# Kernel optimization log

Hardware: AMD Instinct MI355X
Metric: run time of the kernel (lower is better)

The kernel has to match this reference:

```python
import jax, jax.numpy as jnp
import numpy as np

B, D, NSTEPS = 256, 4096, 30
DT = 0.5  # args.dt

def rho(x):
    # hard-sigmoid activation used throughout the EP repo
    return jnp.clip(x, 0.0, 1.0)

def setup_inputs() -> dict:
    key = jax.random.key(0)
    k_s3, k_w0, k_w2, k_w4 = jax.random.split(key, 4)
    sc = 1.0 / np.sqrt(D)
    W0 = jax.random.normal(k_w0, (D, D), jnp.float32) * sc  # w[0]: layer1 -> layer0
    W2 = jax.random.normal(k_w2, (D, D), jnp.float32) * sc  # w[2]: layer2 -> layer1
    W4 = jax.random.normal(k_w4, (D, D), jnp.float32) * sc  # w[4]: data  -> layer2
    return {
        "s0": jnp.zeros((B, D), jnp.float32),
        "s1": jnp.zeros((B, D), jnp.float32),
        "s2": jnp.zeros((B, D), jnp.float32),
        "s3": jax.random.uniform(k_s3, (B, D), jnp.float32),  # clamped data layer in [0,1]
        "W0": W0, "b0": jnp.zeros((D,), jnp.float32),
        "W1": W0.T,  # w[2i+1].weight = w[2i].weight.T at init (tied transpose)
        "W2": W2, "b2": jnp.zeros((D,), jnp.float32),
        "W3": W2.T,
        "W4": W4, "b4": jnp.zeros((D,), jnp.float32),
        "N": NSTEPS,
    }

def reference(s0, s1, s2, s3, W0, b0, W1, W2, b2, W3, W4, b4, N):
    # non-spiking EP free-phase relaxation (beta=0), no_clamp=False
    top_in = rho(s3) @ W4.T + b4  # s3 is clamped data; constant across steps

    def step(carry, _):
        c0, c1, c2 = carry
        r0, r1, r2 = rho(c0), rho(c1), rho(c2)
        ds0 = -c0 + r1 @ W0.T + b0
        ds1 = -c1 + r2 @ W2.T + b2 + r0 @ W1.T
        ds2 = -c2 + top_in + r1 @ W3.T
        n0 = jnp.clip(c0 + DT * ds0, 0.0, 1.0)
        n1 = jnp.clip(c1 + DT * ds1, 0.0, 1.0)
        n2 = jnp.clip(c2 + DT * ds2, 0.0, 1.0)
        return (n0, n1, n2), None

    (s0, s1, s2), _ = jax.lax.scan(step, (s0, s1, s2), None, length=N)
    return jnp.stack([s0, s1, s2])  # [3, B, D]
```

## Files before the change

kernel.cpp:

```cpp
#include <hip/hip_runtime.h>


typedef unsigned short u16;
typedef __attribute__((ext_vector_type(8))) _Float16 f16x8;
typedef __attribute__((ext_vector_type(4))) float f32x4;

constexpr int Bb = 256, Dd = 4096, NSTEPS = 30;
constexpr long BD = (long)Bb * Dd;
constexpr long DD = (long)Dd * Dd;
constexpr int BM = 32;
constexpr int NBUF = 3;
constexpr int BUFB = 20480;

__device__ inline u16 f2h(float f) { union { _Float16 h; u16 u; } v; v.h = (_Float16)f; return v.u; }
__device__ inline float h2f(u16 b) { union { u16 u; _Float16 h; } v; v.u = b; return (float)v.h; }

__device__ inline void gl_lds16(const u16* g, void* l) {
    __builtin_amdgcn_global_load_lds(
        (const __attribute__((address_space(1))) void*)g,
        (__attribute__((address_space(3))) void*)l, 16, 0, 0);
}

__global__ __launch_bounds__(256)
void convert_w(const float* __restrict__ src, u16* __restrict__ dst, long n) {
    long i = (long)blockIdx.x * blockDim.x + threadIdx.x;
    const long stride = (long)gridDim.x * blockDim.x;
    for (long v = i; v < (n >> 2); v += stride) {
        float4 x = ((const float4*)src)[v];
        ushort4 o; o.x = f2h(x.x); o.y = f2h(x.y); o.z = f2h(x.z); o.w = f2h(x.w);
        ((ushort4*)dst)[v] = o;
    }
}

__global__ __launch_bounds__(256)
void convert_s(const float* __restrict__ src, u16* __restrict__ hi, u16* __restrict__ lo, long n) {
    long i = (long)blockIdx.x * blockDim.x + threadIdx.x;
    const long stride = (long)gridDim.x * blockDim.x;
    for (long v = i; v < (n >> 2); v += stride) {
        float4 x = ((const float4*)src)[v];
        float a[4] = {x.x, x.y, x.z, x.w};
        ushort4 oh, ol;
        u16* ph = (u16*)&oh; u16* pl = (u16*)&ol;
        #pragma unroll
        for (int j = 0; j < 4; ++j) {
            float c = fminf(fmaxf(a[j], 0.f), 1.f);
            u16 hb = f2h(c);
            ph[j] = hb;
            pl[j] = f2h(c - h2f(hb));
        }
        ((ushort4*)hi)[v] = oh;
        ((ushort4*)lo)[v] = ol;
    }
}

template<bool WIDE>
__device__ inline void stage_tile(const u16* aH, const u16* aL, const u16* W,
                                  int m0, int n0, int k, char* buf, int wv, int lane)
{
    const int srow = lane >> 2;
    const int koff = (((lane & 3) ^ ((lane >> 3) & 3)) << 3);
    const u16* aBase = (wv < 2) ? aH : aL;
    const int aRow = ((wv & 1) << 4) + srow;
    char* aDst = buf + ((wv >> 1) << 11) + ((wv & 1) << 10);
    gl_lds16(aBase + (size_t)(m0 + aRow) * Dd + k + koff, aDst);
    constexpr int WR = WIDE ? 64 : 32;
    const u16* wSrc = W + (size_t)(n0 + WR * wv + srow) * Dd + k + koff;
    char* wDst = buf + 4096 + wv * (WIDE ? 4096 : 2048);
    #pragma unroll
    for (int c = 0; c < (WIDE ? 4 : 2); ++c)
        gl_lds16(wSrc + (size_t)(16 * c) * Dd, wDst + (c << 10));
}

template<int MODE, bool WIDE>
__device__ inline void run_gemm(const u16* aH0, const u16* aL0, const u16* W0p,
                                const u16* aH1, const u16* aL1, const u16* W1p,
                                const int npass, const int m0, const int n0, char* smem,
                                const float* bias, const float* add,
                                const float* pF, const u16* pH, const u16* pL,
                                float* outF, u16* oH, u16* oL, const long zOff)
{
    const int lane = threadIdx.x & 63, wv = threadIdx.x >> 6;
    constexpr int NJ = WIDE ? 4 : 2;
    f32x4 acc[2][NJ] = {};
    const int nk = npass << 7;

    stage_tile<WIDE>(aH0, aL0, W0p, m0, n0, 0,  smem,        wv, lane);
    stage_tile<WIDE>(aH0, aL0, W0p, m0, n0, 32, smem + BUFB, wv, lane);

    int ib = 0;
    const int r16 = lane & 15;
    const int qoff = (((lane >> 4) ^ ((r16 >> 1) & 3)) << 4);

    for (int kk = 0; kk < nk; ++kk) {
        if (kk + 1 < nk) {
            if (WIDE) asm volatile("s_waitcnt vmcnt(5)" ::: "memory");
            else      asm volatile("s_waitcnt vmcnt(3)" ::: "memory");
        } else {
            asm volatile("s_waitcnt vmcnt(0)" ::: "memory");
        }
        __builtin_amdgcn_s_barrier();
        asm volatile("" ::: "memory");

        const int kk2 = kk + 2;
        if (kk2 < nk) {
            int ib2 = ib + 2; if (ib2 >= NBUF) ib2 -= NBUF;
            const bool p1 = kk2 >= 128;
            stage_tile<WIDE>(p1 ? aH1 : aH0, p1 ? aL1 : aL0, p1 ? W1p : W0p,
                             m0, n0, (kk2 & 127) << 5, smem + ib2 * BUFB, wv, lane);
        }

        const char* buf = smem + ib * BUFB;
        ++ib; if (ib == NBUF) ib = 0;

        f16x8 ah[2], al[2], wf[NJ];
        #pragma unroll
        for (int i = 0; i < 2; ++i) {
            ah[i] = *(const f16x8*)(buf + ((16 * i + r16) << 6) + qoff);
            al[i] = *(const f16x8*)(buf + 2048 + ((16 * i + r16) << 6) + qoff);
        }
        #pragma unroll
        for (int j = 0; j < NJ; ++j)
            wf[j] = *(const f16x8*)(buf + 4096 +
                        (((WIDE ? 64 : 32) * wv + 16 * j + r16) << 6) + qoff);

        __builtin_amdgcn_s_setprio(1);
        #pragma unroll
        for (int j = 0; j < NJ; ++j) {
            #pragma unroll
            for (int i = 0; i < 2; ++i) {
                acc[i][j] = __builtin_amdgcn_mfma_f32_16x16x32_f16(ah[i], wf[j], acc[i][j], 0, 0, 0);
                acc[i][j] = __builtin_amdgcn_mfma_f32_16x16x32_f16(al[i], wf[j], acc[i][j], 0, 0, 0);
            }
        }
        __builtin_amdgcn_s_setprio(0);
    }

    const int q = lane >> 4;
    #pragma unroll
    for (int j = 0; j < NJ; ++j) {
        const int n = n0 + (WIDE ? 64 : 32) * wv + 16 * j + r16;
        #pragma unroll
        for (int i = 0; i < 2; ++i) {
            #pragma unroll
            for (int r = 0; r < 4; ++r) {
                const int m = m0 + 16 * i + q * 4 + r;
                const size_t idx = (size_t)m * Dd + n;
                float e = acc[i][j][r];
                if (MODE == 0) {
                    outF[idx] = e + bias[n];
                } else {
                    if (bias) e += bias[n];
                    if (add)  e += add[idx];
                    const float p = pF ? pF[zOff + idx] : (h2f(pH[zOff + idx]) + h2f(pL[zOff + idx]));
                    float v = 0.5f * p + 0.5f * e;
                    v = fminf(fmaxf(v, 0.f), 1.f);
                    const u16 hb = f2h(v);
                    oH[zOff + idx] = hb;
                    oL[zOff + idx] = f2h(v - h2f(hb));
                    if (outF) outF[zOff + idx] = v;
                }
            }
        }
    }
}

template<int MODE>
__global__ __launch_bounds__(256, 2)
void step_mfma(const u16* __restrict__ sH, const u16* __restrict__ sL,
               const u16* __restrict__ W0h, const u16* __restrict__ W1h,
               const u16* __restrict__ W2h, const u16* __restrict__ W3h,
               const float* __restrict__ b0, const float* __restrict__ b2,
               const float* __restrict__ top,
               const float* __restrict__ pF,
               const u16* __restrict__ pH, const u16* __restrict__ pL,
               float* __restrict__ outF,
               u16* __restrict__ oH, u16* __restrict__ oL)
{
    __shared__ __align__(16) char smem[NBUF * BUFB];
    const int id = blockIdx.x;

    if (MODE == 0) {
        const int mt = id >> 5, nt = id & 31;
        run_gemm<0, false>(sH, sL, W0h, nullptr, nullptr, nullptr, 1,
                           mt * BM, nt * 128, smem, b0, nullptr,
                           nullptr, nullptr, nullptr, outF, nullptr, nullptr, 0);
    } else {
        if (id < 128) {
            const int mt = id >> 4, nt = id & 15;
            run_gemm<1, true>(sH + BD, sL + BD, W0h, nullptr, nullptr, nullptr, 1,
                              mt * BM, nt * 256, smem, b0, nullptr,
                              pF, pH, pL, outF, oH, oL, 0);
        } else if (id < 384) {
            const int t = id - 128, mt = t >> 5, nt = t & 31;
            run_gemm<1, false>(sH + 2 * BD, sL + 2 * BD, W2h, sH, sL, W1h, 2,
                               mt * BM, nt * 128, smem, b2, nullptr,
                               pF, pH, pL, outF, oH, oL, BD);
        } else {
            const int t = id - 384, mt = t >> 4, nt = t & 15;
            run_gemm<1, true>(sH + BD, sL + BD, W3h, nullptr, nullptr, nullptr, 1,
                              mt * BM, nt * 256, smem, nullptr, top,
                              pF, pH, pL, outF, oH, oL, 2 * BD);
        }
    }
}

extern "C" void kernel_launch(void* const* d_in, const int* in_sizes, int n_in,
                              void* d_out, int out_size, void* d_ws, size_t ws_size,
                              hipStream_t stream)
{
    const float* s0 = (const float*)d_in[0];
    const float* s1 = (const float*)d_in[1];
    const float* s2 = (const float*)d_in[2];
    const float* s3 = (const float*)d_in[3];
    const float* W0 = (const float*)d_in[4];
    const float* b0 = (const float*)d_in[5];
    const float* W1 = (const float*)d_in[6];
    const float* W2 = (const float*)d_in[7];
    const float* b2 = (const float*)d_in[8];
    const float* W3 = (const float*)d_in[9];
    const float* W4 = (const float*)d_in[10];
    const float* b4 = (const float*)d_in[11];

    float* top = (float*)d_ws;
    u16* u   = (u16*)(top + BD);
    u16* W0h = u;            u16* W1h = u + DD;     u16* W2h = u + 2 * DD;
    u16* W3h = u + 3 * DD;   u16* W4h = u + 4 * DD;
    u16* sHa = u + 5 * DD;
    u16* sLa = sHa + 3 * BD;
    u16* sHb = sLa + 3 * BD;
    u16* sLb = sHb + 3 * BD;
    u16* s3h = sLb + 3 * BD;
    u16* s3l = s3h + BD;

    float* out = (float*)d_out;
    const dim3 blk(256);
    const dim3 cgrid(512);

    convert_w<<<cgrid, blk, 0, stream>>>(W0, W0h, DD);
    convert_w<<<cgrid, blk, 0, stream>>>(W1, W1h, DD);
    convert_w<<<cgrid, blk, 0, stream>>>(W2, W2h, DD);
    convert_w<<<cgrid, blk, 0, stream>>>(W3, W3h, DD);
    convert_w<<<cgrid, blk, 0, stream>>>(W4, W4h, DD);
    convert_s<<<cgrid, blk, 0, stream>>>(s3, s3h, s3l, BD);
    convert_s<<<cgrid, blk, 0, stream>>>(s0, sHa,          sLa,          BD);
    convert_s<<<cgrid, blk, 0, stream>>>(s1, sHa + BD,     sLa + BD,     BD);
    convert_s<<<cgrid, blk, 0, stream>>>(s2, sHa + 2 * BD, sLa + 2 * BD, BD);

    step_mfma<0><<<dim3(256), blk, 0, stream>>>(
        s3h, s3l, W4h, nullptr, nullptr, nullptr,
        b4, nullptr, nullptr,
        nullptr, nullptr, nullptr,
        top, nullptr, nullptr);

    for (int t = 0; t < NSTEPS; ++t) {
        const u16* iH = (t & 1) ? sHb : sHa;
        const u16* iL = (t & 1) ? sLb : sLa;
        u16*       vH = (t & 1) ? sHa : sHb;
        u16*       vL = (t & 1) ? sLa : sLb;
        float* oF = (t == NSTEPS - 1) ? out : nullptr;
        if (t == 0) {
            hipMemcpyAsync(out,          s0, BD * sizeof(float), hipMemcpyDeviceToDevice, stream);
            hipMemcpyAsync(out + BD,     s1, BD * sizeof(float), hipMemcpyDeviceToDevice, stream);
            hipMemcpyAsync(out + 2 * BD, s2, BD * sizeof(float), hipMemcpyDeviceToDevice, stream);
            step_mfma<1><<<dim3(512), blk, 0, stream>>>(
                iH, iL, W0h, W1h, W2h, W3h, b0, b2, top,
                out, nullptr, nullptr,
                oF, vH, vL);
        } else {
            step_mfma<1><<<dim3(512), blk, 0, stream>>>(
                iH, iL, W0h, W1h, W2h, W3h, b0, b2, top,
                nullptr, iH, iL,
                oF, vH, vL);
        }
    }
}
```

Before: 3.760 ms.

## Split layer-1 two-pass GEMM into two wide tiles with separate finish kernel

The layer-1 update, which needed a K=8192 two-pass GEMM over narrow 128-column tiles, is split into two independent K=4096 GEMMs on wide 256-column tiles that write fp32 partials. A new elementwise kernel sums the partials and applies the update, clamp and hi/lo split. All blocks now do equal work, which removes the long tail from the double-length layer-1 blocks, and the wider tiles reuse the A operand more. In exchange it adds a kernel launch per step plus extra global traffic for the partials. The partials reuse the W4 conversion buffer as scratch, and the top-input GEMM now also uses wide tiles.

```diff
diff --git a/kernel.cpp b/kernel.cpp
--- a/kernel.cpp
+++ b/kernel.cpp
@@ -53,7 +53,6 @@
     }
 }
 
-template<bool WIDE>
 __device__ inline void stage_tile(const u16* aH, const u16* aL, const u16* W,
                                   int m0, int n0, int k, char* buf, int wv, int lane)
 {
@@ -63,69 +62,58 @@
     const int aRow = ((wv & 1) << 4) + srow;
     char* aDst = buf + ((wv >> 1) << 11) + ((wv & 1) << 10);
     gl_lds16(aBase + (size_t)(m0 + aRow) * Dd + k + koff, aDst);
-    constexpr int WR = WIDE ? 64 : 32;
-    const u16* wSrc = W + (size_t)(n0 + WR * wv + srow) * Dd + k + koff;
-    char* wDst = buf + 4096 + wv * (WIDE ? 4096 : 2048);
+    const u16* wSrc = W + (size_t)(n0 + 64 * wv + srow) * Dd + k + koff;
+    char* wDst = buf + 4096 + wv * 4096;
     #pragma unroll
-    for (int c = 0; c < (WIDE ? 4 : 2); ++c)
+    for (int c = 0; c < 4; ++c)
         gl_lds16(wSrc + (size_t)(16 * c) * Dd, wDst + (c << 10));
 }
 
-template<int MODE, bool WIDE>
-__device__ inline void run_gemm(const u16* aH0, const u16* aL0, const u16* W0p,
-                                const u16* aH1, const u16* aL1, const u16* W1p,
-                                const int npass, const int m0, const int n0, char* smem,
+template<bool FULL>
+__device__ inline void run_gemm(const u16* aH, const u16* aL, const u16* W,
+                                const int m0, const int n0, char* smem,
                                 const float* bias, const float* add,
                                 const float* pF, const u16* pH, const u16* pL,
                                 float* outF, u16* oH, u16* oL, const long zOff)
 {
     const int lane = threadIdx.x & 63, wv = threadIdx.x >> 6;
-    constexpr int NJ = WIDE ? 4 : 2;
-    f32x4 acc[2][NJ] = {};
-    const int nk = npass << 7;
-
-    stage_tile<WIDE>(aH0, aL0, W0p, m0, n0, 0,  smem,        wv, lane);
-    stage_tile<WIDE>(aH0, aL0, W0p, m0, n0, 32, smem + BUFB, wv, lane);
+    f32x4 acc[2][4] = {};
+    constexpr int nk = 128;
+
+    stage_tile(aH, aL, W, m0, n0, 0,  smem,        wv, lane);
+    stage_tile(aH, aL, W, m0, n0, 32, smem + BUFB, wv, lane);
 
     int ib = 0;
     const int r16 = lane & 15;
     const int qoff = (((lane >> 4) ^ ((r16 >> 1) & 3)) << 4);
 
     for (int kk = 0; kk < nk; ++kk) {
-        if (kk + 1 < nk) {
-            if (WIDE) asm volatile("s_waitcnt vmcnt(5)" ::: "memory");
-            else      asm volatile("s_waitcnt vmcnt(3)" ::: "memory");
-        } else {
-            asm volatile("s_waitcnt vmcnt(0)" ::: "memory");
-        }
+        if (kk + 1 < nk) asm volatile("s_waitcnt vmcnt(5)" ::: "memory");
+        else             asm volatile("s_waitcnt vmcnt(0)" ::: "memory");
         __builtin_amdgcn_s_barrier();
         asm volatile("" ::: "memory");
 
-        const int kk2 = kk + 2;
-        if (kk2 < nk) {
+        if (kk + 2 < nk) {
             int ib2 = ib + 2; if (ib2 >= NBUF) ib2 -= NBUF;
-            const bool p1 = kk2 >= 128;
-            stage_tile<WIDE>(p1 ? aH1 : aH0, p1 ? aL1 : aL0, p1 ? W1p : W0p,
-                             m0, n0, (kk2 & 127) << 5, smem + ib2 * BUFB, wv, lane);
+            stage_tile(aH, aL, W, m0, n0, (kk + 2) << 5, smem + ib2 * BUFB, wv, lane);
         }
 
         const char* buf = smem + ib * BUFB;
         ++ib; if (ib == NBUF) ib = 0;
 
-        f16x8 ah[2], al[2], wf[NJ];
+        f16x8 ah[2], al[2], wf[4];
         #pragma unroll
         for (int i = 0; i < 2; ++i) {
             ah[i] = *(const f16x8*)(buf + ((16 * i + r16) << 6) + qoff);
             al[i] = *(const f16x8*)(buf + 2048 + ((16 * i + r16) << 6) + qoff);
         }
         #pragma unroll
-        for (int j = 0; j < NJ; ++j)
-            wf[j] = *(const f16x8*)(buf + 4096 +
-                        (((WIDE ? 64 : 32) * wv + 16 * j + r16) << 6) + qoff);
+        for (int j = 0; j < 4; ++j)
+            wf[j] = *(const f16x8*)(buf + 4096 + ((64 * wv + 16 * j + r16) << 6) + qoff);
 
         __builtin_amdgcn_s_setprio(1);
         #pragma unroll
-        for (int j = 0; j < NJ; ++j) {
+        for (int j = 0; j < 4; ++j) {
             #pragma unroll
             for (int i = 0; i < 2; ++i) {
                 acc[i][j] = __builtin_amdgcn_mfma_f32_16x16x32_f16(ah[i], wf[j], acc[i][j], 0, 0, 0);
@@ -137,8 +125,8 @@
 
     const int q = lane >> 4;
     #pragma unroll
-    for (int j = 0; j < NJ; ++j) {
-        const int n = n0 + (WIDE ? 64 : 32) * wv + 16 * j + r16;
+    for (int j = 0; j < 4; ++j) {
+        const int n = n0 + 64 * wv + 16 * j + r16;
         #pragma unroll
         for (int i = 0; i < 2; ++i) {
             #pragma unroll
@@ -146,8 +134,8 @@
                 const int m = m0 + 16 * i + q * 4 + r;
                 const size_t idx = (size_t)m * Dd + n;
                 float e = acc[i][j][r];
-                if (MODE == 0) {
-                    outF[idx] = e + bias[n];
+                if (!FULL) {
+                    outF[idx] = bias ? e + bias[n] : e;
                 } else {
                     if (bias) e += bias[n];
                     if (add)  e += add[idx];
@@ -174,34 +162,70 @@
                const float* __restrict__ pF,
                const u16* __restrict__ pH, const u16* __restrict__ pL,
                float* __restrict__ outF,
-               u16* __restrict__ oH, u16* __restrict__ oL)
+               u16* __restrict__ oH, u16* __restrict__ oL,
+               float* __restrict__ p0, float* __restrict__ p1)
 {
     __shared__ __align__(16) char smem[NBUF * BUFB];
     const int id = blockIdx.x;
 
     if (MODE == 0) {
-        const int mt = id >> 5, nt = id & 31;
-        run_gemm<0, false>(sH, sL, W0h, nullptr, nullptr, nullptr, 1,
-                           mt * BM, nt * 128, smem, b0, nullptr,
-                           nullptr, nullptr, nullptr, outF, nullptr, nullptr, 0);
+        const int mt = id >> 4, nt = id & 15;
+        run_gemm<false>(sH, sL, W0h, mt * BM, nt * 256, smem, b0, nullptr,
+                        nullptr, nullptr, nullptr, outF, nullptr, nullptr, 0);
     } else {
+        const int t = id & 127, mt = t >> 4, nt = t & 15;
+        const int m0 = mt * BM, n0 = nt * 256;
         if (id < 128) {
-            const int mt = id >> 4, nt = id & 15;
-            run_gemm<1, true>(sH + BD, sL + BD, W0h, nullptr, nullptr, nullptr, 1,
-                              mt * BM, nt * 256, smem, b0, nullptr,
-                              pF, pH, pL, outF, oH, oL, 0);
+            run_gemm<true>(sH + BD, sL + BD, W0h, m0, n0, smem, b0, nullptr,
+                           pF, pH, pL, outF, oH, oL, 0);
+        } else if (id < 256) {
+            run_gemm<false>(sH + 2 * BD, sL + 2 * BD, W2h, m0, n0, smem, b2, nullptr,
+                            nullptr, nullptr, nullptr, p0, nullptr, nullptr, 0);
         } else if (id < 384) {
-            const int t = id - 128, mt = t >> 5, nt = t & 31;
-            run_gemm<1, false>(sH + 2 * BD, sL + 2 * BD, W2h, sH, sL, W1h, 2,
-                               mt * BM, nt * 128, smem, b2, nullptr,
-                               pF, pH, pL, outF, oH, oL, BD);
+            run_gemm<false>(sH, sL, W1h, m0, n0, smem, nullptr, nullptr,
+                            nullptr, nullptr, nullptr, p1, nullptr, nullptr, 0);
         } else {
-            const int t = id - 384, mt = t >> 4, nt = t & 15;
-            run_gemm<1, true>(sH + BD, sL + BD, W3h, nullptr, nullptr, nullptr, 1,
-                              mt * BM, nt * 256, smem, nullptr, top,
-                              pF, pH, pL, outF, oH, oL, 2 * BD);
-        }
-    }
+            run_gemm<true>(sH + BD, sL + BD, W3h, m0, n0, smem, nullptr, top,
+                           pF, pH, pL, outF, oH, oL, 2 * BD);
+        }
+    }
+}
+
+__global__ __launch_bounds__(256)
+void finish_l1(const float* __restrict__ p0, const float* __restrict__ p1,
+               const float* __restrict__ pF,
+               const u16* __restrict__ pH, const u16* __restrict__ pL,
+               float* __restrict__ outF, u16* __restrict__ oH, u16* __restrict__ oL)
+{
+    const long v = (long)blockIdx.x * blockDim.x + threadIdx.x;
+    float4 a = ((const float4*)p0)[v];
+    float4 b = ((const float4*)p1)[v];
+    float e[4] = {a.x + b.x, a.y + b.y, a.z + b.z, a.w + b.w};
+    float p[4];
+    if (pF) {
+        float4 pv = ((const float4*)(pF + BD))[v];
+        p[0] = pv.x; p[1] = pv.y; p[2] = pv.z; p[3] = pv.w;
+    } else {
+        ushort4 hv = ((const ushort4*)(pH + BD))[v];
+        ushort4 lv = ((const ushort4*)(pL + BD))[v];
+        p[0] = h2f(hv.x) + h2f(lv.x); p[1] = h2f(hv.y) + h2f(lv.y);
+        p[2] = h2f(hv.z) + h2f(lv.z); p[3] = h2f(hv.w) + h2f(lv.w);
+    }
+    ushort4 oh, ol; u16* ph = (u16*)&oh; u16* pl = (u16*)&ol;
+    float4 ov;
+    float* po = (float*)&ov;
+    #pragma unroll
+    for (int j = 0; j < 4; ++j) {
+        float x = 0.5f * p[j] + 0.5f * e[j];
+        x = fminf(fmaxf(x, 0.f), 1.f);
+        const u16 hb = f2h(x);
+        ph[j] = hb;
+        pl[j] = f2h(x - h2f(hb));
+        po[j] = x;
+    }
+    ((ushort4*)(oH + BD))[v] = oh;
+    ((ushort4*)(oL + BD))[v] = ol;
+    if (outF) ((float4*)(outF + BD))[v] = ov;
 }
 
 extern "C" void kernel_launch(void* const* d_in, const int* in_sizes, int n_in,
@@ -231,6 +255,8 @@
     u16* sLb = sHb + 3 * BD;
     u16* s3h = sLb + 3 * BD;
     u16* s3l = s3h + BD;
+    float* p0 = (float*)W4h;
+    float* p1 = p0 + BD;
 
     float* out = (float*)d_out;
     const dim3 blk(256);
@@ -246,11 +272,11 @@
     convert_s<<<cgrid, blk, 0, stream>>>(s1, sHa + BD,     sLa + BD,     BD);
     convert_s<<<cgrid, blk, 0, stream>>>(s2, sHa + 2 * BD, sLa + 2 * BD, BD);
 
-    step_mfma<0><<<dim3(256), blk, 0, stream>>>(
+    step_mfma<0><<<dim3(128), blk, 0, stream>>>(
         s3h, s3l, W4h, nullptr, nullptr, nullptr,
         b4, nullptr, nullptr,
         nullptr, nullptr, nullptr,
-        top, nullptr, nullptr);
+        top, nullptr, nullptr, nullptr, nullptr);
 
     for (int t = 0; t < NSTEPS; ++t) {
         const u16* iH = (t & 1) ? sHb : sHa;
@@ -258,19 +284,18 @@
         u16*       vH = (t & 1) ? sHa : sHb;
         u16*       vL = (t & 1) ? sLa : sLb;
         float* oF = (t == NSTEPS - 1) ? out : nullptr;
+        const float* pF = nullptr;
         if (t == 0) {
             hipMemcpyAsync(out,          s0, BD * sizeof(float), hipMemcpyDeviceToDevice, stream);
             hipMemcpyAsync(out + BD,     s1, BD * sizeof(float), hipMemcpyDeviceToDevice, stream);
             hipMemcpyAsync(out + 2 * BD, s2, BD * sizeof(float), hipMemcpyDeviceToDevice, stream);
-            step_mfma<1><<<dim3(512), blk, 0, stream>>>(
-                iH, iL, W0h, W1h, W2h, W3h, b0, b2, top,
-                out, nullptr, nullptr,
-                oF, vH, vL);
-        } else {
-            step_mfma<1><<<dim3(512), blk, 0, stream>>>(
-                iH, iL, W0h, W1h, W2h, W3h, b0, b2, top,
-                nullptr, iH, iL,
-                oF, vH, vL);
-        }
-    }
-}
+            pF = out;
+        }
+        step_mfma<1><<<dim3(512), blk, 0, stream>>>(
+            iH, iL, W0h, W1h, W2h, W3h, b0, b2, top,
+            pF, iH, iL,
+            oF, vH, vL, p0, p1);
+        finish_l1<<<dim3(BD / 4 / 256), blk, 0, stream>>>(
+            p0, p1, pF, iH, iL, oF, vH, vL);
+    }
+}
```

Measured after the change: 3.758 ms. About the same (-0.1%).
